# Optimization experiments

Measured on AMD Instinct MI355X. Metric: run time of the kernel, lower is better.

Reference implementation:

```python
import jax, jax.numpy as jnp
import numpy as np

WIN = 7
ATTN_AREA = WIN * WIN  # 49
NUM_HEADS = 16
C = 512
B = 2048


def _relative_position_index(win_h, win_w):
    coords = np.stack(np.meshgrid(np.arange(win_h), np.arange(win_w), indexing='ij'))  # [2,h,w]
    flat = coords.reshape(2, -1)                      # [2, h*w]
    rel = flat[:, :, None] - flat[:, None, :]         # [2, N, N]
    rel = rel.transpose(1, 2, 0).copy()               # [N, N, 2]
    rel[:, :, 0] += win_h - 1
    rel[:, :, 1] += win_w - 1
    rel[:, :, 0] *= 2 * win_w - 1
    return rel.sum(-1).astype(np.int32)               # [N, N]


def setup_inputs() -> dict:
    key = jax.random.key(0)
    ks = jax.random.split(key, 8)
    s = 0.02
    return {
        'x': jax.random.normal(ks[0], (B, ATTN_AREA, C), dtype=jnp.float32),
        'w_qkv': jax.random.normal(ks[1], (3 * C, C), dtype=jnp.float32) * s,
        'b_qkv': jax.random.normal(ks[2], (3 * C,), dtype=jnp.float32) * s,
        'w_gamma': jax.random.normal(ks[3], (C, C), dtype=jnp.float32) * s,
        'b_gamma': jax.random.normal(ks[4], (C,), dtype=jnp.float32) * s,
        'w_proj': jax.random.normal(ks[5], (C, C), dtype=jnp.float32) * s,
        'b_proj': jax.random.normal(ks[6], (C,), dtype=jnp.float32) * s,
        'bias_table': jax.random.normal(ks[7], ((2 * WIN - 1) * (2 * WIN - 1), NUM_HEADS), dtype=jnp.float32) * s,
        'rel_idx': jnp.asarray(_relative_position_index(WIN, WIN)),
    }


def reference(x, w_qkv, b_qkv, w_gamma, b_gamma, w_proj, b_proj, bias_table, rel_idx):
    B_, N, Cdim = x.shape
    H = NUM_HEADS
    hd = Cdim // H
    scale = H ** (-0.5)  # NOTE: module scales by num_heads**-0.5, kept faithful

    qkv = x @ w_qkv.T + b_qkv                              # [B, N, 3C]
    qkv = qkv.reshape(B_, N, 3, H, hd).transpose(2, 0, 3, 1, 4)  # [3, B, H, N, hd]
    q, k, v = qkv[0] * scale, qkv[1], qkv[2]

    # gathered relative-position bias: [H, N, N]
    bias = bias_table[rel_idx.reshape(-1)].reshape(N, N, H).transpose(2, 0, 1)

    scores = jnp.einsum('bhid,bhjd->bhij', q, k) + bias[None]  # [B, H, N, N]
    attn = jax.nn.softmax(scores, axis=-1)
    out = jnp.einsum('bhij,bhjd->bhid', attn, v)               # [B, H, N, hd]
    out = out.transpose(0, 2, 1, 3).reshape(B_, N, Cdim)

    out = out @ w_gamma.T + b_gamma   # LipNorm gamma linear
    out = out @ w_proj.T + b_proj
    return out
```

## Files before the change

kernel.cpp:

```cpp
#include <hip/hip_runtime.h>
#include <hip/hip_bf16.h>
#include <stdint.h>

typedef __hip_bfloat16 bf16;
typedef __bf16 bf16x8 __attribute__((ext_vector_type(8)));
typedef float f32x4 __attribute__((ext_vector_type(4)));

__device__ __forceinline__ f32x4 mfma_bf16(bf16x8 a, bf16x8 b, f32x4 c) {
    return __builtin_amdgcn_mfma_f32_16x16x32_bf16(a, b, c, 0, 0, 0);
}

__device__ __forceinline__ void gload16(const bf16* g, bf16* l) {
    __builtin_amdgcn_global_load_lds(
        (const __attribute__((address_space(1))) uint32_t*)g,
        (__attribute__((address_space(3))) uint32_t*)l, 16, 0, 0);
}

__global__ __launch_bounds__(256) void cvt_f32_bf16(const float* __restrict__ s,
                                                    bf16* __restrict__ d, long n4) {
    long i = (long)blockIdx.x * 256 + threadIdx.x;
    if (i >= n4) return;
    const float4 v = ((const float4*)s)[i];
    union { bf16 h[4]; uint2 u; } o;
    o.h[0] = __float2bfloat16(v.x);
    o.h[1] = __float2bfloat16(v.y);
    o.h[2] = __float2bfloat16(v.z);
    o.h[3] = __float2bfloat16(v.w);
    ((uint2*)d)[i] = o.u;
}


__global__ __launch_bounds__(256) void prep_bias(const float* __restrict__ bt,
                                                 const int* __restrict__ rel,
                                                 float* __restrict__ biasF) {
    int t = blockIdx.x * 256 + threadIdx.x;
    if (t >= 16 * 2401) return;
    int h = t / 2401;
    int rem = t - h * 2401;
    biasF[t] = bt[rel[rem] * 16 + h];
}

__global__ __launch_bounds__(256) void prep_wc(const float* __restrict__ Wg,
                                               const float* __restrict__ bg,
                                               const float* __restrict__ Wp,
                                               const float* __restrict__ bp,
                                               bf16* __restrict__ Wc,
                                               float* __restrict__ bc) {
    __shared__ float wp[512];
    const int n = blockIdx.x;
    const int t = threadIdx.x;
    wp[t]       = Wp[n * 512 + t];
    wp[t + 256] = Wp[n * 512 + t + 256];
    __syncthreads();
    for (int c = t; c < 512; c += 256) {
        float s = 0.f;
        for (int j = 0; j < 512; j++) s += wp[j] * Wg[j * 512 + c];
        Wc[n * 512 + c] = __float2bfloat16(s);
    }
    if (t == 0) {
        float s = 0.f;
        for (int j = 0; j < 512; j++) s += wp[j] * bg[j];
        bc[n] = s + bp[n];
    }
}


__device__ __forceinline__ void stage_tiles(const bf16* gA, const bf16* gB, int k0,
                                            bf16* AS, bf16* BS, int tid) {
    gload16(gA + k0, AS + tid * 8);
    gload16(gA + 64 * 512 + k0, AS + tid * 8 + 2048);
    gload16(gB + k0, BS + tid * 8);
    gload16(gB + 64 * 512 + k0, BS + tid * 8 + 2048);
}

__device__ __forceinline__ void compute_step(const bf16* AS, const bf16* BS,
                                             int wr, int wc, int l15, int q4,
                                             f32x4 acc[4][4]) {
    bf16x8 af[4], bfv[4];
#pragma unroll
    for (int i = 0; i < 4; i++)
        af[i] = *(const bf16x8*)(AS + (wr * 64 + i * 16 + l15) * 32 + q4 * 8);
#pragma unroll
    for (int i = 0; i < 4; i++)
        bfv[i] = *(const bf16x8*)(BS + (wc * 64 + i * 16 + l15) * 32 + q4 * 8);
#pragma unroll
    for (int mi = 0; mi < 4; mi++)
#pragma unroll
        for (int ni = 0; ni < 4; ni++)
            acc[mi][ni] = mfma_bf16(af[mi], bfv[ni], acc[mi][ni]);
}

template <int MODE>
__global__ __launch_bounds__(256, 3) void gemm_bt(const bf16* __restrict__ A,
                                                  const bf16* __restrict__ Bw,
                                                  const float* __restrict__ bias,
                                                  bf16* __restrict__ O0,
                                                  bf16* __restrict__ O1,
                                                  bf16* __restrict__ O2,
                                                  float* __restrict__ Of,
                                                  int nTilesN) {
    __shared__ __align__(16) bf16 As0[128 * 32];
    __shared__ __align__(16) bf16 As1[128 * 32];
    __shared__ __align__(16) bf16 Bs0[128 * 32];
    __shared__ __align__(16) bf16 Bs1[128 * 32];

    const int tid  = threadIdx.x;
    const int lane = tid & 63;
    const int l15  = lane & 15;
    const int q4   = lane >> 4;
    const int wave = tid >> 6;
    const int wr   = wave >> 1, wc = wave & 1;

    const int nwg = gridDim.x;
    const int qq  = nwg >> 3, rr = nwg & 7;
    const int xcd = blockIdx.x & 7, lin = blockIdx.x >> 3;
    const int wg  = (xcd < rr ? xcd * (qq + 1) : rr * (qq + 1) + (xcd - rr) * qq) + lin;

    const int  tn = wg % nTilesN;
    const long tm = wg / nTilesN;

    const int srow = tid >> 2;
    const int scol = (tid & 3) * 8;
    const bf16* gA = A + (tm * 128 + srow) * 512 + scol;
    const bf16* gB = Bw + ((long)tn * 128 + srow) * 512 + scol;

    const f32x4 z4 = {0.f, 0.f, 0.f, 0.f};
    f32x4 acc[4][4];
#pragma unroll
    for (int i = 0; i < 4; i++)
#pragma unroll
        for (int j = 0; j < 4; j++) acc[i][j] = z4;

    stage_tiles(gA, gB, 0, As0, Bs0, tid);
    __syncthreads();

    for (int k0 = 0; k0 < 512; k0 += 64) {
        stage_tiles(gA, gB, k0 + 32, As1, Bs1, tid);
        compute_step(As0, Bs0, wr, wc, l15, q4, acc);
        __syncthreads();
        if (k0 + 64 < 512) stage_tiles(gA, gB, k0 + 64, As0, Bs0, tid);
        compute_step(As1, Bs1, wr, wc, l15, q4, acc);
        __syncthreads();
    }

    const int colb = tn * 128 + wc * 64;
    const int rowb = (int)(tm * 128) + wr * 64;
#pragma unroll
    for (int mi = 0; mi < 4; mi++) {
#pragma unroll
        for (int ni = 0; ni < 4; ni++) {
            const int   col = colb + ni * 16 + l15;
            const float bv  = bias[col];
            if (MODE == 0) {
                const int which = col >> 9;
                const int h     = (col >> 5) & 15;
                const int d     = col & 31;
#pragma unroll
                for (int r = 0; r < 4; r++) {
                    const unsigned row = rowb + mi * 16 + q4 * 4 + r;
                    const unsigned b   = row / 49u;
                    const int      tok = (int)(row - b * 49u);
                    const long     bh  = (long)b * 16 + h;
                    const float    v   = acc[mi][ni][r] + bv;
                    if (which == 0)
                        O0[bh * 1568 + tok * 32 + d] = __float2bfloat16(v * 0.25f);
                    else if (which == 1)
                        O1[bh * 1568 + tok * 32 + d] = __float2bfloat16(v);
                    else
                        O2[bh * 2048 + (long)d * 64 + tok] = __float2bfloat16(v);
                }
            } else {
#pragma unroll
                for (int r = 0; r < 4; r++) {
                    const long row = (long)rowb + mi * 16 + q4 * 4 + r;
                    Of[row * 512 + col] = acc[mi][ni][r] + bv;
                }
            }
        }
    }
}

__global__ __launch_bounds__(64) void attn_kernel(const bf16* __restrict__ Qg,
                                                  const bf16* __restrict__ Kg,
                                                  const bf16* __restrict__ Vg,
                                                  const float* __restrict__ bF,
                                                  bf16* __restrict__ AO) {
    __shared__ __align__(16) char smem[12288];
    bf16* sQ = (bf16*)smem;
    bf16* sK = (bf16*)(smem + 4096);
    bf16* sP = (bf16*)smem;
    bf16* sV = (bf16*)(smem + 8192);

    const int bh   = blockIdx.x;
    const int b    = bh >> 4, h = bh & 15;
    const int lane = threadIdx.x;
    const int l15  = lane & 15, q4 = lane >> 4;

    {
        const uint4* gq  = (const uint4*)(Qg + (long)bh * 1568);
        const uint4* gk  = (const uint4*)(Kg + (long)bh * 1568);
        const uint4* gv  = (const uint4*)(Vg + (long)bh * 2048);
        uint4*       q4p = (uint4*)sQ;
        uint4*       k4p = (uint4*)sK;
        uint4*       v4p = (uint4*)sV;
#pragma unroll
        for (int i = 0; i < 3; i++) {
            q4p[lane + 64 * i] = gq[lane + 64 * i];
            k4p[lane + 64 * i] = gk[lane + 64 * i];
        }
        if (lane < 4) {
            q4p[192 + lane] = gq[192 + lane];
            k4p[192 + lane] = gk[192 + lane];
        }
        if (lane < 60) {
            const uint4 z = {0u, 0u, 0u, 0u};
            q4p[196 + lane] = z;
            k4p[196 + lane] = z;
        }
#pragma unroll
        for (int i = 0; i < 4; i++) v4p[lane + 64 * i] = gv[lane + 64 * i];
    }
    __syncthreads();

    const f32x4 z4 = {0.f, 0.f, 0.f, 0.f};
    f32x4 s[4][4];
    {
        bf16x8 aq[4], bk[4];
#pragma unroll
        for (int i = 0; i < 4; i++)
            aq[i] = *(const bf16x8*)(sQ + (i * 16 + l15) * 32 + q4 * 8);
#pragma unroll
        for (int i = 0; i < 4; i++)
            bk[i] = *(const bf16x8*)(sK + (i * 16 + l15) * 32 + q4 * 8);
#pragma unroll
        for (int mi = 0; mi < 4; mi++)
#pragma unroll
            for (int ni = 0; ni < 4; ni++) s[mi][ni] = mfma_bf16(aq[mi], bk[ni], z4);
    }
    __syncthreads();

    const float* bFh = bF + h * 2401;
#pragma unroll
    for (int mi = 0; mi < 4; mi++) {
#pragma unroll
        for (int r = 0; r < 4; r++) {
            const int  row  = mi * 16 + q4 * 4 + r;
            const bool vrow = row < 49;
            float p[4];
            float sum = 0.f;
#pragma unroll
            for (int ni = 0; ni < 4; ni++) {
                const int col = ni * 16 + l15;
                float sv;
                if (col < 49 && vrow)
                    sv = s[mi][ni][r] + bFh[row * 49 + col];
                else
                    sv = -1e30f;
                p[ni] = __expf(sv);
                sum += p[ni];
            }
#pragma unroll
            for (int msk = 1; msk <= 8; msk <<= 1) sum += __shfl_xor(sum, msk);
            const float inv = vrow ? (1.f / sum) : 0.f;
#pragma unroll
            for (int ni = 0; ni < 4; ni++)
                sP[row * 64 + ni * 16 + l15] = __float2bfloat16(p[ni] * inv);
        }
    }
    __syncthreads();

    f32x4 o[4][2];
#pragma unroll
    for (int i = 0; i < 4; i++)
#pragma unroll
        for (int j = 0; j < 2; j++) o[i][j] = z4;
#pragma unroll
    for (int ks = 0; ks < 2; ks++) {
        bf16x8 ap[4], bv[2];
#pragma unroll
        for (int mi = 0; mi < 4; mi++)
            ap[mi] = *(const bf16x8*)(sP + (mi * 16 + l15) * 64 + ks * 32 + q4 * 8);
#pragma unroll
        for (int ni = 0; ni < 2; ni++)
            bv[ni] = *(const bf16x8*)(sV + (ni * 16 + l15) * 64 + ks * 32 + q4 * 8);
#pragma unroll
        for (int mi = 0; mi < 4; mi++)
#pragma unroll
            for (int ni = 0; ni < 2; ni++) o[mi][ni] = mfma_bf16(ap[mi], bv[ni], o[mi][ni]);
    }

    bf16* aout = AO + (long)b * 49 * 512 + h * 32;
#pragma unroll
    for (int mi = 0; mi < 4; mi++)
#pragma unroll
        for (int ni = 0; ni < 2; ni++)
#pragma unroll
            for (int r = 0; r < 4; r++) {
                const int tok = mi * 16 + q4 * 4 + r;
                if (tok < 49) aout[tok * 512 + ni * 16 + l15] = __float2bfloat16(o[mi][ni][r]);
            }
}


extern "C" void kernel_launch(void* const* d_in, const int* in_sizes, int n_in,
                              void* d_out, int out_size, void* d_ws, size_t ws_size,
                              hipStream_t stream) {
    const float* x    = (const float*)d_in[0];
    const float* wqkv = (const float*)d_in[1];
    const float* bqkv = (const float*)d_in[2];
    const float* wg   = (const float*)d_in[3];
    const float* bg   = (const float*)d_in[4];
    const float* wp   = (const float*)d_in[5];
    const float* bp   = (const float*)d_in[6];
    const float* btab = (const float*)d_in[7];
    const int*   ridx = (const int*)d_in[8];
    float*       out  = (float*)d_out;

    char* ws = (char*)d_ws;
    float* bF  = (float*)ws;
    bf16*  Wcc = (bf16*)(ws + 163840);
    float* bcc = (float*)(ws + 688128);
    bf16*  Wqb = (bf16*)(ws + 690176);
    const long HDR = 2263040;

    int nchunks = 16;
    for (int n = 1; n <= 16; n *= 2) {
        long W = 2048 / n;
        if (HDR + W * 266240L <= (long)ws_size) { nchunks = n; break; }
    }
    const long W = 2048 / nchunks;
    char* p = ws + HDR;
    bf16* Xb = (bf16*)p;  p += W * 50176;
    bf16* Q  = (bf16*)p;  p += W * 50176;
    bf16* Kk = (bf16*)p;  p += W * 50176;
    bf16* Vt = (bf16*)p;  p += W * 65536;
    bf16* AO = (bf16*)p;

    prep_bias<<<151, 256, 0, stream>>>(btab, ridx, bF);
    prep_wc<<<512, 256, 0, stream>>>(wg, bg, wp, bp, Wcc, bcc);
    cvt_f32_bf16<<<(1536 * 512 / 4 + 255) / 256, 256, 0, stream>>>(wqkv, Wqb, 1536 * 512 / 4);

    const long M = W * 49;
    const long n4x = M * 512 / 4;
    for (int c = 0; c < nchunks; c++) {
        const long off = (long)c * M * 512;
        cvt_f32_bf16<<<(int)((n4x + 255) / 256), 256, 0, stream>>>(x + off, Xb, n4x);
        gemm_bt<0><<<(int)(M / 128) * 12, 256, 0, stream>>>(
            Xb, Wqb, bqkv, Q, Kk, Vt, nullptr, 12);
        attn_kernel<<<(int)(W * 16), 64, 0, stream>>>(Q, Kk, Vt, bF, AO);
        gemm_bt<1><<<(int)(M / 128) * 4, 256, 0, stream>>>(
            AO, Wcc, bcc, nullptr, nullptr, nullptr, out + off, 4);
    }
}
```

Before: 1.028 ms.

## Enlarge GEMM tiles to 256x256 with 8 waves, swizzled LDS and explicit scheduling

Result: slower. 1.057 ms (+2.8%).

```diff
diff --git a/kernel.cpp b/kernel.cpp
--- a/kernel.cpp
+++ b/kernel.cpp
@@ -64,34 +64,8 @@
     }
 }
 
-
-__device__ __forceinline__ void stage_tiles(const bf16* gA, const bf16* gB, int k0,
-                                            bf16* AS, bf16* BS, int tid) {
-    gload16(gA + k0, AS + tid * 8);
-    gload16(gA + 64 * 512 + k0, AS + tid * 8 + 2048);
-    gload16(gB + k0, BS + tid * 8);
-    gload16(gB + 64 * 512 + k0, BS + tid * 8 + 2048);
-}
-
-__device__ __forceinline__ void compute_step(const bf16* AS, const bf16* BS,
-                                             int wr, int wc, int l15, int q4,
-                                             f32x4 acc[4][4]) {
-    bf16x8 af[4], bfv[4];
-#pragma unroll
-    for (int i = 0; i < 4; i++)
-        af[i] = *(const bf16x8*)(AS + (wr * 64 + i * 16 + l15) * 32 + q4 * 8);
-#pragma unroll
-    for (int i = 0; i < 4; i++)
-        bfv[i] = *(const bf16x8*)(BS + (wc * 64 + i * 16 + l15) * 32 + q4 * 8);
-#pragma unroll
-    for (int mi = 0; mi < 4; mi++)
-#pragma unroll
-        for (int ni = 0; ni < 4; ni++)
-            acc[mi][ni] = mfma_bf16(af[mi], bfv[ni], acc[mi][ni]);
-}
-
 template <int MODE>
-__global__ __launch_bounds__(256, 3) void gemm_bt(const bf16* __restrict__ A,
+__global__ __launch_bounds__(512, 2) void gemm_bt(const bf16* __restrict__ A,
                                                   const bf16* __restrict__ Bw,
                                                   const float* __restrict__ bias,
                                                   bf16* __restrict__ O0,
@@ -99,17 +73,15 @@
                                                   bf16* __restrict__ O2,
                                                   float* __restrict__ Of,
                                                   int nTilesN) {
-    __shared__ __align__(16) bf16 As0[128 * 32];
-    __shared__ __align__(16) bf16 As1[128 * 32];
-    __shared__ __align__(16) bf16 Bs0[128 * 32];
-    __shared__ __align__(16) bf16 Bs1[128 * 32];
+    __shared__ __align__(16) bf16 sm[2][2][256 * 32];
 
     const int tid  = threadIdx.x;
     const int lane = tid & 63;
     const int l15  = lane & 15;
     const int q4   = lane >> 4;
     const int wave = tid >> 6;
-    const int wr   = wave >> 1, wc = wave & 1;
+    const int wr   = wave >> 2;
+    const int wc   = wave & 3;
 
     const int nwg = gridDim.x;
     const int qq  = nwg >> 3, rr = nwg & 7;
@@ -119,34 +91,113 @@
     const int  tn = wg % nTilesN;
     const long tm = wg / nTilesN;
 
-    const int srow = tid >> 2;
-    const int scol = (tid & 3) * 8;
-    const bf16* gA = A + (tm * 128 + srow) * 512 + scol;
-    const bf16* gB = Bw + ((long)tn * 128 + srow) * 512 + scol;
+    const bf16* gA = A + tm * 256 * 512;
+    const bf16* gB = Bw + (long)tn * 256 * 512;
+
+    int srcOff[2], dstOff[2];
+#pragma unroll
+    for (int l = 0; l < 2; l++) {
+        const int idx = l * 512 + tid;
+        const int row = idx >> 2, p = idx & 3;
+        const int c   = p ^ ((row >> 1) & 3);
+        srcOff[l] = row * 512 + c * 8;
+        dstOff[l] = idx * 8;
+    }
+
+    int offA[8], offB[4];
+#pragma unroll
+    for (int mi = 0; mi < 8; mi++) {
+        const int row = wr * 128 + mi * 16 + l15;
+        offA[mi] = row * 32 + (q4 ^ ((row >> 1) & 3)) * 8;
+    }
+#pragma unroll
+    for (int ni = 0; ni < 4; ni++) {
+        const int row = wc * 64 + ni * 16 + l15;
+        offB[ni] = row * 32 + (q4 ^ ((row >> 1) & 3)) * 8;
+    }
 
     const f32x4 z4 = {0.f, 0.f, 0.f, 0.f};
-    f32x4 acc[4][4];
-#pragma unroll
-    for (int i = 0; i < 4; i++)
+    f32x4 acc[8][4];
+#pragma unroll
+    for (int i = 0; i < 8; i++)
 #pragma unroll
         for (int j = 0; j < 4; j++) acc[i][j] = z4;
 
-    stage_tiles(gA, gB, 0, As0, Bs0, tid);
-    __syncthreads();
-
-    for (int k0 = 0; k0 < 512; k0 += 64) {
-        stage_tiles(gA, gB, k0 + 32, As1, Bs1, tid);
-        compute_step(As0, Bs0, wr, wc, l15, q4, acc);
-        __syncthreads();
-        if (k0 + 64 < 512) stage_tiles(gA, gB, k0 + 64, As0, Bs0, tid);
-        compute_step(As1, Bs1, wr, wc, l15, q4, acc);
-        __syncthreads();
-    }
-
-    const int colb = tn * 128 + wc * 64;
-    const int rowb = (int)(tm * 128) + wr * 64;
-#pragma unroll
-    for (int mi = 0; mi < 4; mi++) {
+    {
+        bf16* dA = &sm[0][0][0];
+        bf16* dB = &sm[0][1][0];
+        gload16(gA + srcOff[0], dA + dstOff[0]);
+        gload16(gA + srcOff[1], dA + dstOff[1]);
+        gload16(gB + srcOff[0], dB + dstOff[0]);
+        gload16(gB + srcOff[1], dB + dstOff[1]);
+    }
+    asm volatile("s_waitcnt vmcnt(0)" ::: "memory");
+    __builtin_amdgcn_sched_barrier(0);
+    __builtin_amdgcn_s_barrier();
+    __builtin_amdgcn_sched_barrier(0);
+
+#pragma unroll 2
+    for (int t = 0; t < 16; t++) {
+        const int b = t & 1;
+        const bf16* As = &sm[b][0][0];
+        const bf16* Bs = &sm[b][1][0];
+
+        bf16x8 bfv[4], af[4];
+#pragma unroll
+        for (int ni = 0; ni < 4; ni++) bfv[ni] = *(const bf16x8*)(Bs + offB[ni]);
+#pragma unroll
+        for (int mi = 0; mi < 4; mi++) af[mi] = *(const bf16x8*)(As + offA[mi]);
+        if (t < 15) {
+            const int k0 = (t + 1) * 32;
+            bf16* dA = &sm[b ^ 1][0][0];
+            bf16* dB = &sm[b ^ 1][1][0];
+            gload16(gA + k0 + srcOff[0], dA + dstOff[0]);
+            gload16(gA + k0 + srcOff[1], dA + dstOff[1]);
+            gload16(gB + k0 + srcOff[0], dB + dstOff[0]);
+            gload16(gB + k0 + srcOff[1], dB + dstOff[1]);
+        }
+        __builtin_amdgcn_s_barrier();
+        __builtin_amdgcn_sched_barrier(0);
+        asm volatile("s_waitcnt lgkmcnt(0)" ::: "memory");
+        __builtin_amdgcn_sched_barrier(0);
+        __builtin_amdgcn_s_setprio(1);
+#pragma unroll
+        for (int mi = 0; mi < 4; mi++)
+#pragma unroll
+            for (int ni = 0; ni < 4; ni++)
+                acc[mi][ni] = mfma_bf16(af[mi], bfv[ni], acc[mi][ni]);
+        __builtin_amdgcn_s_setprio(0);
+        __builtin_amdgcn_sched_barrier(0);
+        __builtin_amdgcn_s_barrier();
+        __builtin_amdgcn_sched_barrier(0);
+
+        bf16x8 ag[4];
+#pragma unroll
+        for (int mi = 0; mi < 4; mi++) ag[mi] = *(const bf16x8*)(As + offA[4 + mi]);
+        __builtin_amdgcn_s_barrier();
+        __builtin_amdgcn_sched_barrier(0);
+        asm volatile("s_waitcnt lgkmcnt(0)" ::: "memory");
+        __builtin_amdgcn_sched_barrier(0);
+        __builtin_amdgcn_s_setprio(1);
+#pragma unroll
+        for (int mi = 0; mi < 4; mi++)
+#pragma unroll
+            for (int ni = 0; ni < 4; ni++)
+                acc[4 + mi][ni] = mfma_bf16(ag[mi], bfv[ni], acc[4 + mi][ni]);
+        __builtin_amdgcn_s_setprio(0);
+        __builtin_amdgcn_sched_barrier(0);
+        if (t < 15) {
+            asm volatile("s_waitcnt vmcnt(0)" ::: "memory");
+        }
+        __builtin_amdgcn_sched_barrier(0);
+        __builtin_amdgcn_s_barrier();
+        __builtin_amdgcn_sched_barrier(0);
+    }
+
+    const int colb = tn * 256 + wc * 64;
+    const int rowb = (int)(tm * 256) + wr * 128;
+#pragma unroll
+    for (int mi = 0; mi < 8; mi++) {
 #pragma unroll
         for (int ni = 0; ni < 4; ni++) {
             const int   col = colb + ni * 16 + l15;
@@ -323,8 +374,8 @@
     bf16*  Wqb = (bf16*)(ws + 690176);
     const long HDR = 2263040;
 
-    int nchunks = 16;
-    for (int n = 1; n <= 16; n *= 2) {
+    int nchunks = 8;
+    for (int n = 1; n <= 8; n *= 2) {
         long W = 2048 / n;
         if (HDR + W * 266240L <= (long)ws_size) { nchunks = n; break; }
     }
@@ -345,10 +396,10 @@
     for (int c = 0; c < nchunks; c++) {
         const long off = (long)c * M * 512;
         cvt_f32_bf16<<<(int)((n4x + 255) / 256), 256, 0, stream>>>(x + off, Xb, n4x);
-        gemm_bt<0><<<(int)(M / 128) * 12, 256, 0, stream>>>(
-            Xb, Wqb, bqkv, Q, Kk, Vt, nullptr, 12);
+        gemm_bt<0><<<(int)(M / 256) * 6, 512, 0, stream>>>(
+            Xb, Wqb, bqkv, Q, Kk, Vt, nullptr, 6);
         attn_kernel<<<(int)(W * 16), 64, 0, stream>>>(Q, Kk, Vt, bF, AO);
-        gemm_bt<1><<<(int)(M / 128) * 4, 256, 0, stream>>>(
-            AO, Wcc, bcc, nullptr, nullptr, nullptr, out + off, 4);
-    }
-}
+        gemm_bt<1><<<(int)(M / 256) * 2, 512, 0, stream>>>(
+            AO, Wcc, bcc, nullptr, nullptr, nullptr, out + off, 2);
+    }
+}
```

## Use four-stage swizzled LDS pipeline with explicit waitcnt in bf16 GEMM

Applied to the files above, without the earlier changes.

After: 1.022 ms. Within noise of the previous version (-0.6%).

```diff
diff --git a/kernel.cpp b/kernel.cpp
--- a/kernel.cpp
+++ b/kernel.cpp
@@ -64,34 +64,8 @@
     }
 }
 
-
-__device__ __forceinline__ void stage_tiles(const bf16* gA, const bf16* gB, int k0,
-                                            bf16* AS, bf16* BS, int tid) {
-    gload16(gA + k0, AS + tid * 8);
-    gload16(gA + 64 * 512 + k0, AS + tid * 8 + 2048);
-    gload16(gB + k0, BS + tid * 8);
-    gload16(gB + 64 * 512 + k0, BS + tid * 8 + 2048);
-}
-
-__device__ __forceinline__ void compute_step(const bf16* AS, const bf16* BS,
-                                             int wr, int wc, int l15, int q4,
-                                             f32x4 acc[4][4]) {
-    bf16x8 af[4], bfv[4];
-#pragma unroll
-    for (int i = 0; i < 4; i++)
-        af[i] = *(const bf16x8*)(AS + (wr * 64 + i * 16 + l15) * 32 + q4 * 8);
-#pragma unroll
-    for (int i = 0; i < 4; i++)
-        bfv[i] = *(const bf16x8*)(BS + (wc * 64 + i * 16 + l15) * 32 + q4 * 8);
-#pragma unroll
-    for (int mi = 0; mi < 4; mi++)
-#pragma unroll
-        for (int ni = 0; ni < 4; ni++)
-            acc[mi][ni] = mfma_bf16(af[mi], bfv[ni], acc[mi][ni]);
-}
-
 template <int MODE>
-__global__ __launch_bounds__(256, 3) void gemm_bt(const bf16* __restrict__ A,
+__global__ __launch_bounds__(256, 2) void gemm_bt(const bf16* __restrict__ A,
                                                   const bf16* __restrict__ Bw,
                                                   const float* __restrict__ bias,
                                                   bf16* __restrict__ O0,
@@ -99,10 +73,7 @@
                                                   bf16* __restrict__ O2,
                                                   float* __restrict__ Of,
                                                   int nTilesN) {
-    __shared__ __align__(16) bf16 As0[128 * 32];
-    __shared__ __align__(16) bf16 As1[128 * 32];
-    __shared__ __align__(16) bf16 Bs0[128 * 32];
-    __shared__ __align__(16) bf16 Bs1[128 * 32];
+    __shared__ __align__(16) bf16 sm[4][2][128 * 32];
 
     const int tid  = threadIdx.x;
     const int lane = tid & 63;
@@ -119,10 +90,30 @@
     const int  tn = wg % nTilesN;
     const long tm = wg / nTilesN;
 
-    const int srow = tid >> 2;
-    const int scol = (tid & 3) * 8;
-    const bf16* gA = A + (tm * 128 + srow) * 512 + scol;
-    const bf16* gB = Bw + ((long)tn * 128 + srow) * 512 + scol;
+    const bf16* gA = A + tm * 128 * 512;
+    const bf16* gB = Bw + (long)tn * 128 * 512;
+
+    int srcOff[2], dstOff[2];
+#pragma unroll
+    for (int l = 0; l < 2; l++) {
+        const int idx = l * 256 + tid;
+        const int row = idx >> 2, p = idx & 3;
+        const int c   = p ^ ((row >> 1) & 3);
+        srcOff[l] = row * 512 + c * 8;
+        dstOff[l] = idx * 8;
+    }
+
+    int offA[4], offB[4];
+#pragma unroll
+    for (int mi = 0; mi < 4; mi++) {
+        const int row = wr * 64 + mi * 16 + l15;
+        offA[mi] = row * 32 + (q4 ^ ((row >> 1) & 3)) * 8;
+    }
+#pragma unroll
+    for (int ni = 0; ni < 4; ni++) {
+        const int row = wc * 64 + ni * 16 + l15;
+        offB[ni] = row * 32 + (q4 ^ ((row >> 1) & 3)) * 8;
+    }
 
     const f32x4 z4 = {0.f, 0.f, 0.f, 0.f};
     f32x4 acc[4][4];
@@ -131,17 +122,54 @@
 #pragma unroll
         for (int j = 0; j < 4; j++) acc[i][j] = z4;
 
-    stage_tiles(gA, gB, 0, As0, Bs0, tid);
-    __syncthreads();
-
-    for (int k0 = 0; k0 < 512; k0 += 64) {
-        stage_tiles(gA, gB, k0 + 32, As1, Bs1, tid);
-        compute_step(As0, Bs0, wr, wc, l15, q4, acc);
-        __syncthreads();
-        if (k0 + 64 < 512) stage_tiles(gA, gB, k0 + 64, As0, Bs0, tid);
-        compute_step(As1, Bs1, wr, wc, l15, q4, acc);
-        __syncthreads();
-    }
+#define STAGE(t)                                                    \
+    do {                                                            \
+        const int k0_ = (t) * 32;                                   \
+        bf16* dA_ = &sm[(t) & 3][0][0];                             \
+        bf16* dB_ = &sm[(t) & 3][1][0];                             \
+        gload16(gA + k0_ + srcOff[0], dA_ + dstOff[0]);             \
+        gload16(gA + k0_ + srcOff[1], dA_ + dstOff[1]);             \
+        gload16(gB + k0_ + srcOff[0], dB_ + dstOff[0]);             \
+        gload16(gB + k0_ + srcOff[1], dB_ + dstOff[1]);             \
+    } while (0)
+
+    STAGE(0);
+    STAGE(1);
+    STAGE(2);
+
+#pragma unroll
+    for (int t = 0; t < 16; t++) {
+        if (t <= 13)
+            asm volatile("s_waitcnt vmcnt(8)" ::: "memory");
+        else if (t == 14)
+            asm volatile("s_waitcnt vmcnt(4)" ::: "memory");
+        else
+            asm volatile("s_waitcnt vmcnt(0)" ::: "memory");
+        __builtin_amdgcn_sched_barrier(0);
+        __builtin_amdgcn_s_barrier();
+        __builtin_amdgcn_sched_barrier(0);
+
+        const bf16* As = &sm[t & 3][0][0];
+        const bf16* Bs = &sm[t & 3][1][0];
+        bf16x8 af[4], bfv[4];
+#pragma unroll
+        for (int mi = 0; mi < 4; mi++) af[mi] = *(const bf16x8*)(As + offA[mi]);
+#pragma unroll
+        for (int ni = 0; ni < 4; ni++) bfv[ni] = *(const bf16x8*)(Bs + offB[ni]);
+        if (t + 3 < 16) STAGE(t + 3);
+        __builtin_amdgcn_sched_barrier(0);
+        asm volatile("s_waitcnt lgkmcnt(0)" ::: "memory");
+        __builtin_amdgcn_sched_barrier(0);
+        __builtin_amdgcn_s_setprio(1);
+#pragma unroll
+        for (int mi = 0; mi < 4; mi++)
+#pragma unroll
+            for (int ni = 0; ni < 4; ni++)
+                acc[mi][ni] = mfma_bf16(af[mi], bfv[ni], acc[mi][ni]);
+        __builtin_amdgcn_s_setprio(0);
+        __builtin_amdgcn_sched_barrier(0);
+    }
+#undef STAGE
 
     const int colb = tn * 128 + wc * 64;
     const int rowb = (int)(tm * 128) + wr * 64;
@@ -324,7 +352,7 @@
     const long HDR = 2263040;
 
     int nchunks = 16;
-    for (int n = 1; n <= 16; n *= 2) {
+    for (int n = 4; n <= 16; n *= 2) {
         long W = 2048 / n;
         if (HDR + W * 266240L <= (long)ws_size) { nchunks = n; break; }
     }
```
